# Performance work log

Hardware: AMD Instinct MI355X
Metric: run time of the kernel (lower is better)

Reference implementation:

```python
import jax, jax.numpy as jnp
import numpy as np

SIZE = 128
RATIO = 0.5

def setup_inputs() -> dict:
    key = jax.random.key(0)
    k1, k2, k3 = jax.random.split(key, 3)
    B, D, K = 16, 256, 18
    assp_features = jax.random.normal(k1, (B, D, SIZE, SIZE), dtype=jnp.float32)
    prototypes = jax.random.normal(k2, (B, K, D), dtype=jnp.float32)
    n_samp = int(SIZE * SIZE * RATIO)
    # sample without replacement, matching np.random.choice(replace=False)
    random_indices = jax.random.permutation(k3, SIZE * SIZE)[:n_samp].astype(jnp.int64)
    return {"assp_features": assp_features, "prototypes": prototypes,
            "random_indices": random_indices}

def reference(assp_features, prototypes, random_indices):
    # assp_features: [B, D, H, W], prototypes: [B, K, D], random_indices: [N]
    size = assp_features.shape[-1]
    x = random_indices // size  # [N]
    y = random_indices % size   # [N]
    f = assp_features[:, :, x, y]            # [B, D, N] gathered pixel features
    # squared L2 distances [B, N, K]; argmin of ||p-f||_2 == argmin of squared dist
    p2 = jnp.sum(prototypes * prototypes, axis=-1)       # [B, K]
    f2 = jnp.sum(f * f, axis=1)                          # [B, N]
    cross = jnp.einsum('bdn,bkd->bnk', f, prototypes)    # [B, N, K]
    d2 = p2[:, None, :] - 2.0 * cross + f2[:, :, None]
    idx = jnp.argmin(d2, axis=-1)                        # [B, N]
    nearest = jnp.take_along_axis(prototypes, idx[..., None], axis=1)  # [B, N, D]
    out = assp_features.at[:, :, x, y].set(jnp.swapaxes(nearest, 1, 2))
    return out
```

## Files before the change

kernel.cpp:

```cpp
#include <hip/hip_runtime.h>

constexpr int B = 16;
constexpr int D = 256;
constexpr int K = 18;
constexpr int SZ = 128;
constexpr int S = SZ * SZ;
constexpr int N = S / 2;

__global__ __launch_bounds__(512) void prep_kernel(
    const float* __restrict__ proto,
    const int* __restrict__ idx,
    unsigned char* __restrict__ mask,
    double* __restrict__ p2) {
  for (int i = threadIdx.x; i < S; i += 512) mask[i] = 0;
  __syncthreads();
  for (int n = threadIdx.x; n < N; n += 512) mask[idx[n]] = 1;

  for (int i = threadIdx.x; i < B * K; i += 512) {
    const float4* p = (const float4*)(proto + (size_t)i * D);
    double s0 = 0, s1 = 0, s2 = 0, s3 = 0;
#pragma unroll 4
    for (int q = 0; q < D / 4; ++q) {
      const float4 v = p[q];
      s0 += (double)v.x * (double)v.x;
      s1 += (double)v.y * (double)v.y;
      s2 += (double)v.z * (double)v.z;
      s3 += (double)v.w * (double)v.w;
    }
    p2[i] = (s0 + s1) + (s2 + s3);
  }
}

__global__ __launch_bounds__(256) void argmin_kernel(
    const float* __restrict__ assp,
    const float* __restrict__ proto,
    const double* __restrict__ p2,
    const unsigned char* __restrict__ mask,
    signed char* __restrict__ table) {
  __shared__ double spd[D][K];

  const int b     = blockIdx.x & 15;
  const int chunk = blockIdx.x >> 4;

  const float* pb = proto + (size_t)b * K * D;
  for (int i = threadIdx.x; i < K * D; i += 256) {
    const int k = i >> 8;
    const int d = i & 255;
    spd[d][k] = (double)pb[i];
  }
  __syncthreads();

  const int s = chunk * 256 + threadIdx.x;
  const float* fb = assp + (size_t)b * D * S + s;

  double acc[K];
#pragma unroll
  for (int k = 0; k < K; ++k) acc[k] = 0.0;

  for (int d = 0; d < D; d += 8) {
    float fv[8];
#pragma unroll
    for (int j = 0; j < 8; ++j)
      fv[j] = fb[(size_t)(d + j) * S];
#pragma unroll
    for (int j = 0; j < 8; ++j) {
      const double f = (double)fv[j];
      const double* pr = spd[d + j];
#pragma unroll
      for (int k = 0; k < K; ++k) acc[k] += f * pr[k];
    }
  }

  const double* p2b = p2 + (size_t)b * K;
  double best = 1e300;
  int bi = 0;
#pragma unroll
  for (int k = 0; k < K; ++k) {
    const double d2 = p2b[k] - 2.0 * acc[k];
    if (d2 < best) { best = d2; bi = k; }
  }

  if (mask[s]) table[(size_t)b * S + s] = (signed char)bi;
}

__global__ __launch_bounds__(256) void scatter_kernel(
    const float* __restrict__ assp,
    const float* __restrict__ proto,
    const signed char* __restrict__ table,
    float* __restrict__ out) {
  const int bd = blockIdx.x;
  const int b  = bd >> 8;
  const int d  = bd & 255;

  __shared__ float sp[K];
  if (threadIdx.x < K)
    sp[threadIdx.x] = proto[((size_t)b * K + threadIdx.x) * D + d];
  __syncthreads();

  const signed char* tb = table + (size_t)b * S;
  const float4* in4 = (const float4*)(assp + (size_t)bd * S);
  float4* out4 = (float4*)(out + (size_t)bd * S);

#pragma unroll
  for (int it = 0; it < S / 4 / 256; ++it) {
    const int i = it * 256 + threadIdx.x;
    char4 t;
    *(int*)&t = ((const int*)tb)[i];
    float4 v = in4[i];
    if (t.x >= 0) v.x = sp[(int)t.x];
    if (t.y >= 0) v.y = sp[(int)t.y];
    if (t.z >= 0) v.z = sp[(int)t.z];
    if (t.w >= 0) v.w = sp[(int)t.w];
    out4[i] = v;
  }
}

extern "C" void kernel_launch(void* const* d_in, const int* in_sizes, int n_in,
                              void* d_out, int out_size, void* d_ws, size_t ws_size,
                              hipStream_t stream) {
  const float* assp  = (const float*)d_in[0];
  const float* proto = (const float*)d_in[1];
  const int*   idx   = (const int*)d_in[2];
  float* out = (float*)d_out;

  signed char*   table = (signed char*)d_ws;
  unsigned char* mask  = (unsigned char*)d_ws + (size_t)B * S;
  double*        p2    = (double*)((char*)d_ws + (size_t)B * S + S);

  hipMemsetAsync(table, 0xFF, (size_t)B * S, stream);

  prep_kernel<<<1, 512, 0, stream>>>(proto, idx, mask, p2);
  argmin_kernel<<<B * (S / 256), 256, 0, stream>>>(assp, proto, p2, mask, table);
  scatter_kernel<<<B * D, 256, 0, stream>>>(assp, proto, table, out);
}
```

Before: 211.6 us.

## Parallelize prep, process two pixels per thread, move mask test to scatter

```diff
diff --git a/kernel.cpp b/kernel.cpp
--- a/kernel.cpp
+++ b/kernel.cpp
@@ -7,27 +7,24 @@
 constexpr int S = SZ * SZ;
 constexpr int N = S / 2;
 
-__global__ __launch_bounds__(512) void prep_kernel(
+__global__ __launch_bounds__(256) void prep2_kernel(
     const float* __restrict__ proto,
     const int* __restrict__ idx,
     unsigned char* __restrict__ mask,
     double* __restrict__ p2) {
-  for (int i = threadIdx.x; i < S; i += 512) mask[i] = 0;
-  __syncthreads();
-  for (int n = threadIdx.x; n < N; n += 512) mask[idx[n]] = 1;
-
-  for (int i = threadIdx.x; i < B * K; i += 512) {
-    const float4* p = (const float4*)(proto + (size_t)i * D);
-    double s0 = 0, s1 = 0, s2 = 0, s3 = 0;
-#pragma unroll 4
-    for (int q = 0; q < D / 4; ++q) {
-      const float4 v = p[q];
-      s0 += (double)v.x * (double)v.x;
-      s1 += (double)v.y * (double)v.y;
-      s2 += (double)v.z * (double)v.z;
-      s3 += (double)v.w * (double)v.w;
-    }
-    p2[i] = (s0 + s1) + (s2 + s3);
+  const int blk = blockIdx.x;
+  if (blk < 32) {
+    mask[idx[blk * 256 + threadIdx.x]] = 1;
+  } else {
+    const int row  = (blk - 32) * 4 + (threadIdx.x >> 6);
+    const int lane = threadIdx.x & 63;
+    const float4 v = *(const float4*)(proto + (size_t)row * D + lane * 4);
+    double s = (double)v.x * (double)v.x + (double)v.y * (double)v.y
+             + (double)v.z * (double)v.z + (double)v.w * (double)v.w;
+#pragma unroll
+    for (int off = 1; off < 64; off <<= 1)
+      s += __shfl_xor(s, off, 64);
+    if (lane == 0) p2[row] = s;
   }
 }
 
@@ -35,7 +32,6 @@
     const float* __restrict__ assp,
     const float* __restrict__ proto,
     const double* __restrict__ p2,
-    const unsigned char* __restrict__ mask,
     signed char* __restrict__ table) {
   __shared__ double spd[D][K];
 
@@ -43,54 +39,61 @@
   const int chunk = blockIdx.x >> 4;
 
   const float* pb = proto + (size_t)b * K * D;
-  for (int i = threadIdx.x; i < K * D; i += 256) {
-    const int k = i >> 8;
-    const int d = i & 255;
-    spd[d][k] = (double)pb[i];
-  }
+  for (int i = threadIdx.x; i < K * D; i += 256)
+    spd[i & 255][i >> 8] = (double)pb[i];
   __syncthreads();
 
-  const int s = chunk * 256 + threadIdx.x;
-  const float* fb = assp + (size_t)b * D * S + s;
+  const int sA = chunk * 512 + threadIdx.x;
+  const float* fA = assp + (size_t)b * D * S + sA;
 
-  double acc[K];
+  double accA[K], accB[K];
 #pragma unroll
-  for (int k = 0; k < K; ++k) acc[k] = 0.0;
+  for (int k = 0; k < K; ++k) { accA[k] = 0.0; accB[k] = 0.0; }
 
   for (int d = 0; d < D; d += 8) {
-    float fv[8];
-#pragma unroll
-    for (int j = 0; j < 8; ++j)
-      fv[j] = fb[(size_t)(d + j) * S];
+    float va[8], vb[8];
 #pragma unroll
     for (int j = 0; j < 8; ++j) {
-      const double f = (double)fv[j];
+      va[j] = fA[(size_t)(d + j) * S];
+      vb[j] = fA[(size_t)(d + j) * S + 256];
+    }
+#pragma unroll
+    for (int j = 0; j < 8; ++j) {
+      const double a  = (double)va[j];
+      const double bb = (double)vb[j];
       const double* pr = spd[d + j];
 #pragma unroll
-      for (int k = 0; k < K; ++k) acc[k] += f * pr[k];
+      for (int k = 0; k < K; ++k) {
+        const double pk = pr[k];
+        accA[k] += a * pk;
+        accB[k] += bb * pk;
+      }
     }
   }
 
   const double* p2b = p2 + (size_t)b * K;
-  double best = 1e300;
-  int bi = 0;
+  double bestA = 1e300, bestB = 1e300;
+  int kA = 0, kB = 0;
 #pragma unroll
   for (int k = 0; k < K; ++k) {
-    const double d2 = p2b[k] - 2.0 * acc[k];
-    if (d2 < best) { best = d2; bi = k; }
+    const double dA = p2b[k] - 2.0 * accA[k];
+    const double dB = p2b[k] - 2.0 * accB[k];
+    if (dA < bestA) { bestA = dA; kA = k; }
+    if (dB < bestB) { bestB = dB; kB = k; }
   }
-
-  if (mask[s]) table[(size_t)b * S + s] = (signed char)bi;
+  table[(size_t)b * S + sA]       = (signed char)kA;
+  table[(size_t)b * S + sA + 256] = (signed char)kB;
 }
 
 __global__ __launch_bounds__(256) void scatter_kernel(
     const float* __restrict__ assp,
     const float* __restrict__ proto,
     const signed char* __restrict__ table,
+    const unsigned char* __restrict__ mask,
     float* __restrict__ out) {
-  const int bd = blockIdx.x;
-  const int b  = bd >> 8;
-  const int d  = bd & 255;
+  const int d  = 255 - (blockIdx.x >> 4);
+  const int b  = blockIdx.x & 15;
+  const int bd = b * D + d;
 
   __shared__ float sp[K];
   if (threadIdx.x < K)
@@ -104,13 +107,14 @@
 #pragma unroll
   for (int it = 0; it < S / 4 / 256; ++it) {
     const int i = it * 256 + threadIdx.x;
-    char4 t;
+    char4 t, m;
     *(int*)&t = ((const int*)tb)[i];
+    *(int*)&m = ((const int*)mask)[i];
     float4 v = in4[i];
-    if (t.x >= 0) v.x = sp[(int)t.x];
-    if (t.y >= 0) v.y = sp[(int)t.y];
-    if (t.z >= 0) v.z = sp[(int)t.z];
-    if (t.w >= 0) v.w = sp[(int)t.w];
+    if (m.x) v.x = sp[(int)t.x];
+    if (m.y) v.y = sp[(int)t.y];
+    if (m.z) v.z = sp[(int)t.z];
+    if (m.w) v.w = sp[(int)t.w];
     out4[i] = v;
   }
 }
@@ -127,9 +131,8 @@
   unsigned char* mask  = (unsigned char*)d_ws + (size_t)B * S;
   double*        p2    = (double*)((char*)d_ws + (size_t)B * S + S);
 
-  hipMemsetAsync(table, 0xFF, (size_t)B * S, stream);
-
-  prep_kernel<<<1, 512, 0, stream>>>(proto, idx, mask, p2);
-  argmin_kernel<<<B * (S / 256), 256, 0, stream>>>(assp, proto, p2, mask, table);
-  scatter_kernel<<<B * D, 256, 0, stream>>>(assp, proto, table, out);
+  hipMemsetAsync(mask, 0, S, stream);
+  prep2_kernel<<<104, 256, 0, stream>>>(proto, idx, mask, p2);
+  argmin_kernel<<<B * (S / 512), 256, 0, stream>>>(assp, proto, p2, table);
+  scatter_kernel<<<B * D, 256, 0, stream>>>(assp, proto, table, mask, out);
 }
```

Result: faster. 187.9 us (-11.2%).
